# Performance work log

Hardware: AMD Instinct MI355X
Metric: run time of the kernel (lower is better)

Reference implementation:

```python
import jax, jax.numpy as jnp
import numpy as np

T, N, C, D, S = 512, 32, 1296, 512, 30
NORM_SCALE = 32.0
NEGINF = -1e9


def setup_inputs() -> dict:
    key = jax.random.key(0)
    k1, k2, k3, k4, k5 = jax.random.split(key, 5)
    feats = jax.random.normal(k1, (T * N, D), dtype=jnp.float32)
    classifier_weight = jax.random.normal(k2, (D, C), dtype=jnp.float32)
    labeling = jax.random.randint(k3, (N, S), 1, C)  # targets cannot be blank(0)
    logit_lgts = (T - jax.random.randint(k4, (N,), 0, 32)).astype(jnp.int32)
    labeling_lgts = (S - jax.random.randint(k5, (N,), 0, 5)).astype(jnp.int32)
    return dict(feats=feats, classifier_weight=classifier_weight,
                labeling=labeling, logit_lgts=logit_lgts, labeling_lgts=labeling_lgts)


def _ctc_loss(log_probs, labels, in_lens, lab_lens):
    # log_probs: (T, N, C); labels: (N, S); blank = 0; reduction = 'sum'
    Tt, Nn, Cc = log_probs.shape
    Ss = labels.shape[1]
    L = 2 * Ss + 1
    # extended labeling: blank, l1, blank, l2, ..., blank  -> (N, L)
    ext = jnp.zeros((Nn, L), dtype=labels.dtype).at[:, 1::2].set(labels)
    # gather per-state log-probs: (T, N, L)
    lp_ext = jnp.take_along_axis(log_probs, jnp.broadcast_to(ext[None], (Tt, Nn, L)), axis=2)
    # skip transition s-2 -> s allowed iff s > 1 and ext[s] != ext[s-2]
    skip_ok = jnp.concatenate(
        [jnp.zeros((Nn, 2), dtype=bool), ext[:, 2:] != ext[:, :-2]], axis=1)
    alpha0 = (jnp.full((Nn, L), NEGINF, dtype=log_probs.dtype)
              .at[:, 0].set(lp_ext[0, :, 0])
              .at[:, 1].set(lp_ext[0, :, 1]))

    def step(alpha, inp):
        lp_t, t = inp  # lp_t: (N, L)
        a1 = alpha
        a2 = jnp.pad(alpha[:, :-1], ((0, 0), (1, 0)), constant_values=NEGINF)
        a3 = jnp.where(skip_ok,
                       jnp.pad(alpha[:, :-2], ((0, 0), (2, 0)), constant_values=NEGINF),
                       NEGINF)
        new = jax.nn.logsumexp(jnp.stack([a1, a2, a3], axis=0), axis=0) + lp_t
        # freeze alpha once t reaches a sample's input length
        alpha = jnp.where((t < in_lens)[:, None], new, alpha)
        return alpha, None

    alpha, _ = jax.lax.scan(step, alpha0, (lp_ext[1:], jnp.arange(1, Tt)))
    Ln = 2 * lab_lens + 1  # (N,)
    last = jnp.take_along_axis(alpha, (Ln - 1)[:, None], axis=1)[:, 0]
    last2 = jnp.take_along_axis(alpha, (Ln - 2)[:, None], axis=1)[:, 0]
    nll = -jnp.logaddexp(last, last2)
    return jnp.sum(nll)


def reference(feats, classifier_weight, labeling, logit_lgts, labeling_lgts):
    # RadialCTC: cosine logits with norm_scale, then CTC on log-softmax.
    w_n = classifier_weight / jnp.linalg.norm(classifier_weight, axis=0, keepdims=True)  # (D, C)
    f_n = feats / jnp.linalg.norm(feats, axis=1, keepdims=True)  # (T*N, D)
    logits = NORM_SCALE * (f_n @ w_n)  # (T*N, C)
    log_probs = jax.nn.log_softmax(logits.reshape(T, N, C), axis=-1)
    return _ctc_loss(log_probs, labeling, logit_lgts, labeling_lgts)
```

## Files before the change

kernel.cpp:

```cpp
#include <hip/hip_runtime.h>
#include <stdint.h>
#include <stddef.h>


typedef _Float16 f16;
typedef _Float16 f16x8 __attribute__((ext_vector_type(8)));
typedef float f32x4 __attribute__((ext_vector_type(4)));
typedef __attribute__((address_space(1))) void* as1_void_ptr;
typedef __attribute__((address_space(3))) void* as3_void_ptr;

#define TT 512
#define NN 32
#define CC 1296
#define DD 512
#define SS 30
#define CP 1408
#define LL 61
#define NORM_SCALE 32.0f
#define LOG2E 1.4426950408889634f
#define LN2   0.6931471805599453f

#define PREP_WBLK (CP / 16)
#define PREP_ZBLK 16
#define PREP_FBLK (TT * NN / 4)

#define GEMM_BLK ((TT * NN / 128) * (CP / 128))
#define MEGA_GC  NN
#define MEGA_BLK (MEGA_GC + GEMM_BLK)

__device__ __forceinline__ float fexp2(float x) { return __builtin_amdgcn_exp2f(x); }
__device__ __forceinline__ float flog2(float x) { return __builtin_amdgcn_logf(x); }

__device__ __forceinline__ double dpp_sr1_zero64(double x) {
    long long b = __double_as_longlong(x);
    int lo = (int)(b & 0xFFFFFFFFLL);
    int hi = (int)(b >> 32);
    int lo2 = __builtin_amdgcn_update_dpp(0, lo, 0x138, 0xF, 0xF, false);
    int hi2 = __builtin_amdgcn_update_dpp(0, hi, 0x138, 0xF, 0xF, false);
    return __longlong_as_double(((long long)hi2 << 32) |
                                (unsigned long long)(unsigned int)lo2);
}
template <int CTRL>
__device__ __forceinline__ int dpp_imax_level(int m) {
    int t = __builtin_amdgcn_update_dpp(0, m, CTRL, 0xF, 0xF, false);
    return m > t ? m : t;
}

__global__ __launch_bounds__(256) void prep_kernel(const float* __restrict__ W,
                                                   const float* __restrict__ feats,
                                                   f16* __restrict__ wt,
                                                   f16* __restrict__ fn,
                                                   float* __restrict__ sumexp) {
    int bx = blockIdx.x, tid = threadIdx.x;
    if (bx < PREP_WBLK) {
        __shared__ float red[256];
        __shared__ float rqs[16];
        int c0 = bx * 16;
        int cl = tid & 15, dg = tid >> 4;
        int c = c0 + cl;
        float ss = 0.f;
        if (c < CC) {
            for (int d = dg; d < DD; d += 16) {
                float v = W[(size_t)d * CC + c];
                ss += v * v;
            }
        }
        red[tid] = ss;
        __syncthreads();
        if (tid < 16) {
            float s2 = 0.f;
            #pragma unroll
            for (int k = 0; k < 16; ++k) s2 += red[tid + 16 * k];
            rqs[tid] = rsqrtf(s2);
        }
        __syncthreads();
        int c_loc = tid >> 4, dl = tid & 15;
        int cc = c0 + c_loc;
        float rq = rqs[c_loc];
        #pragma unroll 4
        for (int it = 0; it < 32; ++it) {
            int d = dl + it * 16;
            float v = (cc < CC) ? W[(size_t)d * CC + cc] * rq : 0.f;
            wt[(size_t)cc * DD + d] = (f16)v;
        }
    } else if (bx < PREP_WBLK + PREP_ZBLK) {
        int zb = bx - PREP_WBLK;
        float4 z = {0.f, 0.f, 0.f, 0.f};
        ((float4*)sumexp)[zb * 256 + tid] = z;
    } else {
        int fb = bx - PREP_WBLK - PREP_ZBLK;
        int wv = (fb * 256 + tid) >> 6;
        int lane = tid & 63;
        const float4* src = (const float4*)(feats + (size_t)wv * DD) + lane * 2;
        float4 a = src[0], b = src[1];
        float ss = a.x*a.x + a.y*a.y + a.z*a.z + a.w*a.w
                 + b.x*b.x + b.y*b.y + b.z*b.z + b.w*b.w;
        #pragma unroll
        for (int off = 32; off; off >>= 1) ss += __shfl_xor(ss, off);
        float r = rsqrtf(ss);
        f16x8 o;
        o[0]=(f16)(a.x*r); o[1]=(f16)(a.y*r); o[2]=(f16)(a.z*r); o[3]=(f16)(a.w*r);
        o[4]=(f16)(b.x*r); o[5]=(f16)(b.y*r); o[6]=(f16)(b.z*r); o[7]=(f16)(b.w*r);
        *(f16x8*)(fn + (size_t)wv * DD + lane * 8) = o;
    }
}

template <int NT>
__device__ __forceinline__ void gather_wave(const f16* __restrict__ A,
                                            const f16* __restrict__ B,
                                            const int* __restrict__ labels,
                                            float* __restrict__ lp_lab,
                                            int n, int rbase, int lane) {
    __builtin_amdgcn_s_setprio(2);
    int lm = lane & 15, hi = lane >> 4;
    int cls0 = (lm == 0) ? 0 : labels[n * SS + lm - 1];
    int cls1 = (lm >= 15) ? 0 : labels[n * SS + lm + 15];
    const f16* pb0 = B + (size_t)cls0 * DD + hi * 8;
    const f16* pb1 = B + (size_t)cls1 * DD + hi * 8;
    const f16* pa0 = A + ((size_t)(rbase + lm) * NN + n) * DD + hi * 8;
    for (int c = 0; c < 4; ++c) {
        f32x4 acc[NT][2];
        #pragma unroll
        for (int i = 0; i < NT; ++i) {
            acc[i][0] = (f32x4){0.f, 0.f, 0.f, 0.f};
            acc[i][1] = (f32x4){0.f, 0.f, 0.f, 0.f};
        }
        const f16* pac = pa0 + (size_t)c * 128 * NN * DD;
        for (int kb = 0; kb < 16; ++kb) {
            f16x8 bf0 = *(const f16x8*)(pb0 + kb * 32);
            f16x8 bf1 = *(const f16x8*)(pb1 + kb * 32);
            #pragma unroll
            for (int i = 0; i < NT; ++i) {
                f16x8 af = *(const f16x8*)(pac + (size_t)(i * 16) * NN * DD + kb * 32);
                acc[i][0] = __builtin_amdgcn_mfma_f32_16x16x32_f16(af, bf0, acc[i][0], 0, 0, 0);
                acc[i][1] = __builtin_amdgcn_mfma_f32_16x16x32_f16(af, bf1, acc[i][1], 0, 0, 0);
            }
        }
        #pragma unroll
        for (int i = 0; i < NT; ++i) {
            #pragma unroll
            for (int jn = 0; jn < 2; ++jn) {
                int jc = jn * 16 + lm;
                if (jc >= 31) continue;
                float4 o;
                o.x = acc[i][jn][0] * (NORM_SCALE * LOG2E);
                o.y = acc[i][jn][1] * (NORM_SCALE * LOG2E);
                o.z = acc[i][jn][2] * (NORM_SCALE * LOG2E);
                o.w = acc[i][jn][3] * (NORM_SCALE * LOG2E);
                *(float4*)&lp_lab[((size_t)n * 31 + jc) * TT
                                  + c * 128 + rbase + i * 16 + hi * 4] = o;
            }
        }
        __syncthreads();
    }
    __builtin_amdgcn_s_setprio(0);
}

__global__ __launch_bounds__(256) void mega_kernel(const f16* __restrict__ A,
                                                   const f16* __restrict__ B,
                                                   const int* __restrict__ labels,
                                                   const int* __restrict__ in_lens,
                                                   const int* __restrict__ lab_lens,
                                                   float* __restrict__ sumexp,
                                                   float* __restrict__ lp_lab,
                                                   double* __restrict__ part) {
    __shared__ __align__(16) f16 sm[8192];
    int bx = blockIdx.x;
    int tid = threadIdx.x;
    int w = tid >> 6, lane = tid & 63;
    int lm = lane & 15, hi = lane >> 4;
    int sw = (lm >> 1) & 3;

    if (bx >= MEGA_GC) {
        int j = bx - MEGA_GC;
        int x = j & 7, rr = j >> 3;
        int bm = x * 16 + (rr & 15);
        int bn = rr >> 4;
        int wm = w >> 1, wn = w & 1;
        f32x4 acc[4][4];
        f32x4 zero = {0.f, 0.f, 0.f, 0.f};
        #pragma unroll
        for (int i = 0; i < 4; ++i)
            #pragma unroll
            for (int jj = 0; jj < 4; ++jj) acc[i][jj] = zero;

        for (int kb = 0; kb < 16; ++kb) {
            #pragma unroll
            for (int p = 0; p < 2; ++p) {
                int s = p * 256 + tid;
                int row = s >> 2;
                int ch = (s & 3) ^ ((row >> 1) & 3);
                const f16* ga = A + (size_t)(bm * 128 + row) * DD + kb * 32 + ch * 8;
                const f16* gb = B + (size_t)(bn * 128 + row) * DD + kb * 32 + ch * 8;
                __builtin_amdgcn_global_load_lds((as1_void_ptr)ga,
                    (as3_void_ptr)&sm[(p * 256 + w * 64) * 8], 16, 0, 0);
                __builtin_amdgcn_global_load_lds((as1_void_ptr)gb,
                    (as3_void_ptr)&sm[4096 + (p * 256 + w * 64) * 8], 16, 0, 0);
            }
            __syncthreads();
            f16x8 af[4], bf[4];
            #pragma unroll
            for (int i = 0; i < 4; ++i)
                af[i] = *(const f16x8*)&sm[(wm * 64 + i * 16 + lm) * 32 + (hi ^ sw) * 8];
            #pragma unroll
            for (int jj = 0; jj < 4; ++jj)
                bf[jj] = *(const f16x8*)&sm[4096 + (wn * 64 + jj * 16 + lm) * 32 + (hi ^ sw) * 8];
            #pragma unroll
            for (int i = 0; i < 4; ++i)
                #pragma unroll
                for (int jj = 0; jj < 4; ++jj)
                    acc[i][jj] = __builtin_amdgcn_mfma_f32_16x16x32_f16(af[i], bf[jj], acc[i][jj], 0, 0, 0);
            __syncthreads();
        }
        #pragma unroll
        for (int i = 0; i < 4; ++i) {
            float rs[4] = {0.f, 0.f, 0.f, 0.f};
            #pragma unroll
            for (int jj = 0; jj < 4; ++jj) {
                int c = bn * 128 + wn * 64 + jj * 16 + lm;
                bool ok = (c < CC);
                #pragma unroll
                for (int r = 0; r < 4; ++r)
                    rs[r] += ok ? fexp2(acc[i][jj][r] * (NORM_SCALE * LOG2E)) : 0.f;
            }
            #pragma unroll
            for (int off = 1; off < 16; off <<= 1) {
                #pragma unroll
                for (int r = 0; r < 4; ++r) rs[r] += __shfl_xor(rs[r], off);
            }
            if (lm == 0) {
                int rowb = bm * 128 + wm * 64 + i * 16 + hi * 4;
                #pragma unroll
                for (int r = 0; r < 4; ++r) atomicAdd(&sumexp[rowb + r], rs[r]);
            }
        }
        return;
    }

    int n = bx;
    if (w > 0) {
        if (w < 3) gather_wave<3>(A, B, labels, lp_lab, n, (w - 1) * 48, lane);
        else       gather_wave<2>(A, B, labels, lp_lab, n, 96, lane);
        return;
    }

    int s = lane;
    bool valid = s < LL;
    int ext = (valid && (s & 1)) ? labels[n * SS + (s >> 1)] : 0;
    int jmap = (valid && (s & 1)) ? ((s >> 1) + 1) : 0;
    int ext2 = __shfl_up(ext, 2);
    double skipd = ((s >= 2) && valid && (ext != ext2)) ? 1.0 : 0.0;
    double sk1 = dpp_sr1_zero64(skipd);
    double sk2 = dpp_sr1_zero64(sk1);
    double kk2 = skipd * sk2;
    int Tin = in_lens[n];
    const float4* g4 = (const float4*)(lp_lab + ((size_t)n * 31 + jmap) * TT);

    double beta = 0.0;
    int Mi = 0;

    auto stepL = [&](float lp) {
        double P = (double)fexp2(lp);
        double b1 = dpp_sr1_zero64(beta);
        double b2 = dpp_sr1_zero64(b1);
        beta = (beta + b1 + b2 * skipd) * P;
    };
    auto step2 = [&](float lp1, float lp2) {
        double q  = (double)fexp2(lp1);
        double P2 = (double)fexp2(lp2);
        double q1 = dpp_sr1_zero64(q);
        double q2 = dpp_sr1_zero64(q1);
        double c1 = q + q1;
        double c2 = fma(skipd, q + q2, q1);
        double c3 = fma(sk1, q1, skipd * q2);
        double c4 = kk2 * q2;
        double b1 = dpp_sr1_zero64(beta);
        double b2 = dpp_sr1_zero64(b1);
        double b3 = dpp_sr1_zero64(b2);
        double b4 = dpp_sr1_zero64(b3);
        double u = fma(c1, b1, q * beta);
        double v = fma(c3, b3, c2 * b2);
        beta = (u + fma(c4, b4, v)) * P2;
    };
    auto renorm = [&]() {
        int h = (int)(__double_as_longlong(beta) >> 32);
        h = dpp_imax_level<0x111>(h);
        h = dpp_imax_level<0x112>(h);
        h = dpp_imax_level<0x114>(h);
        h = dpp_imax_level<0x118>(h);
        int r0 = __builtin_amdgcn_readlane(h, 15);
        int r1 = __builtin_amdgcn_readlane(h, 31);
        int r2 = __builtin_amdgcn_readlane(h, 47);
        int r3 = __builtin_amdgcn_readlane(h, 63);
        int mx = max(max(r0, r1), max(r2, r3));
        int e11 = mx >> 20;
        double scale = __longlong_as_double((long long)(2046 - e11) << 52);
        beta *= scale;
        Mi += e11 - 1023;
    };

    __builtin_amdgcn_s_setprio(3);
    __syncthreads();
    float4 a0 = g4[0], a1 = g4[1];
    float4 pc0 = g4[2], pc1 = g4[3];
    float4 pn0 = g4[4], pn1 = g4[5];
    beta = (s <= 1) ? (double)fexp2(a0.x) : 0.0;

    stepL(a0.y); stepL(a0.z); stepL(a0.w);
    stepL(a1.x); stepL(a1.y); stepL(a1.z); stepL(a1.w);
    renorm();
    int remaining = Tin - 8;
    int g = 2;
    int rn = 0;
    for (int c = 0; c < 4; ++c) {
        if (c > 0) {
            __syncthreads();
            pc0 = g4[g];     pc1 = g4[g + 1];
            pn0 = g4[g + 2]; pn1 = g4[g + 3];
        }
        int gend = 32 * (c + 1);
        while (g + 2 <= gend && remaining >= 8) {
            int i0 = g + 4 > 127 ? 127 : g + 4;
            int i1 = g + 5 > 127 ? 127 : g + 5;
            float4 pp0 = g4[i0], pp1 = g4[i1];
            step2(pc0.x, pc0.y); step2(pc0.z, pc0.w);
            step2(pc1.x, pc1.y); step2(pc1.z, pc1.w);
            rn ^= 1;
            if (!rn) renorm();
            pc0 = pn0; pc1 = pn1; pn0 = pp0; pn1 = pp1;
            remaining -= 8; g += 2;
        }
    }
    if (remaining > 0) stepL(pc0.x);
    if (remaining > 1) stepL(pc0.y);
    if (remaining > 2) stepL(pc0.z);
    if (remaining > 3) stepL(pc0.w);
    if (remaining > 4) stepL(pc1.x);
    if (remaining > 5) stepL(pc1.y);
    if (remaining > 6) stepL(pc1.z);
    __builtin_amdgcn_s_setprio(0);

    int Ln = 2 * lab_lens[n] + 1;
    double last  = __shfl(beta, Ln - 1);
    double last2 = __shfl(beta, Ln - 2);
    double smv = last + last2;
    long long bb = __double_as_longlong(smv);
    int e = (int)(bb >> 52) - 1023;
    double mant = __longlong_as_double((bb & 0xFFFFFFFFFFFFFLL) | (1023LL << 52));
    if (s == 0)
        part[n] = (double)flog2((float)mant) + (double)(e + Mi);
}

__global__ __launch_bounds__(1024) void final_kernel(const float* __restrict__ sumexp,
                                                     const int* __restrict__ in_lens,
                                                     const double* __restrict__ part,
                                                     float* __restrict__ out) {
    int tid = threadIdx.x;
    int v = tid >> 6, lane = tid & 63;
    __shared__ float nl[NN];
    #pragma unroll
    for (int k = 0; k < 2; ++k) {
        int n = v * 2 + k;
        int Tin = in_lens[n];
        double ms = 0.0;
        for (int t = lane; t < Tin; t += 64)
            ms += (double)flog2(sumexp[(size_t)t * NN + n]);
        #pragma unroll
        for (int off = 32; off; off >>= 1) ms += __shfl_xor(ms, off);
        if (lane == 0) nl[n] = (float)(-(part[n] - ms) * LN2);
    }
    __syncthreads();
    if (tid == 0) {
        float t = 0.f;
        for (int i = 0; i < NN; ++i) t += nl[i];
        out[0] = t;
    }
}

extern "C" void kernel_launch(void* const* d_in, const int* in_sizes, int n_in,
                              void* d_out, int out_size, void* d_ws, size_t ws_size,
                              hipStream_t stream) {
    const float* feats        = (const float*)d_in[0];
    const float* W            = (const float*)d_in[1];
    const int*   labeling     = (const int*)d_in[2];
    const int*   logit_lgts   = (const int*)d_in[3];
    const int*   labeling_lgts= (const int*)d_in[4];
    float* out = (float*)d_out;
    char* ws = (char*)d_ws;

    size_t off = 0;
    f16*   wt     = (f16*)(ws + off);   off += (size_t)CP * DD * 2;
    f16*   fn     = (f16*)(ws + off);   off += (size_t)TT * NN * DD * 2;
    float* sumexp = (float*)(ws + off); off += (size_t)TT * NN * 4;
    float* lp_lab = (float*)(ws + off); off += (size_t)NN * 31 * TT * 4;
    double* part  = (double*)(ws + off); off += NN * 8;

    prep_kernel<<<PREP_WBLK + PREP_ZBLK + PREP_FBLK, 256, 0, stream>>>(
        W, feats, wt, fn, sumexp);
    mega_kernel<<<MEGA_BLK, 256, 0, stream>>>(fn, wt, labeling, logit_lgts,
                                              labeling_lgts, sumexp, lp_lab, part);
    final_kernel<<<1, 1024, 0, stream>>>(sumexp, logit_lgts, part, out);

    (void)in_sizes; (void)n_in; (void)out_size; (void)ws_size;
}
```

Baseline: 153.2 us.

## Split CTC recursion into concurrent forward and backward halves meeting at midpoint

The serial CTC alpha recursion over all timesteps now runs on two waves per sample. One wave does the forward pass over t<256 and another does a backward (beta) pass from Tin-1 down to 256; the two are combined by a dot product through shared memory. The gather work shrinks to two waves that process 128-row chunks in the order the two recursions consume them, and the syncs are rearranged to match. This roughly halves the critical serial dependency chain, at the cost of more complex synchronisation and a second scaled recursion that has to be renormalised.

```diff
diff --git a/kernel.cpp b/kernel.cpp
--- a/kernel.cpp
+++ b/kernel.cpp
@@ -40,10 +40,39 @@
     return __longlong_as_double(((long long)hi2 << 32) |
                                 (unsigned long long)(unsigned int)lo2);
 }
+__device__ __forceinline__ double dpp_sl1_zero64(double x) {
+    long long b = __double_as_longlong(x);
+    int lo = (int)(b & 0xFFFFFFFFLL);
+    int hi = (int)(b >> 32);
+    int lo2 = __builtin_amdgcn_update_dpp(0, lo, 0x130, 0xF, 0xF, false);
+    int hi2 = __builtin_amdgcn_update_dpp(0, hi, 0x130, 0xF, 0xF, false);
+    return __longlong_as_double(((long long)hi2 << 32) |
+                                (unsigned long long)(unsigned int)lo2);
+}
+__device__ __forceinline__ float dpp_sl1_zero32(float x) {
+    int r = __builtin_amdgcn_update_dpp(0, __float_as_int(x), 0x130, 0xF, 0xF, false);
+    return __int_as_float(r);
+}
 template <int CTRL>
 __device__ __forceinline__ int dpp_imax_level(int m) {
     int t = __builtin_amdgcn_update_dpp(0, m, CTRL, 0xF, 0xF, false);
     return m > t ? m : t;
+}
+__device__ __forceinline__ void renorm_d(double& x, int& Mi) {
+    int h = (int)(__double_as_longlong(x) >> 32);
+    h = dpp_imax_level<0x111>(h);
+    h = dpp_imax_level<0x112>(h);
+    h = dpp_imax_level<0x114>(h);
+    h = dpp_imax_level<0x118>(h);
+    int r0 = __builtin_amdgcn_readlane(h, 15);
+    int r1 = __builtin_amdgcn_readlane(h, 31);
+    int r2 = __builtin_amdgcn_readlane(h, 47);
+    int r3 = __builtin_amdgcn_readlane(h, 63);
+    int mx = max(max(r0, r1), max(r2, r3));
+    int e11 = mx >> 20;
+    double scale = __longlong_as_double((long long)(2046 - e11) << 52);
+    x *= scale;
+    Mi += e11 - 1023;
 }
 
 __global__ __launch_bounds__(256) void prep_kernel(const float* __restrict__ W,
@@ -106,54 +135,44 @@
 }
 
 template <int NT>
-__device__ __forceinline__ void gather_wave(const f16* __restrict__ A,
-                                            const f16* __restrict__ B,
-                                            const int* __restrict__ labels,
-                                            float* __restrict__ lp_lab,
-                                            int n, int rbase, int lane) {
-    __builtin_amdgcn_s_setprio(2);
+__device__ __forceinline__ void gather_chunk(const f16* __restrict__ pb0,
+                                             const f16* __restrict__ pb1,
+                                             const f16* __restrict__ A,
+                                             float* __restrict__ lp_lab,
+                                             int n, int c, int rbase, int lane) {
     int lm = lane & 15, hi = lane >> 4;
-    int cls0 = (lm == 0) ? 0 : labels[n * SS + lm - 1];
-    int cls1 = (lm >= 15) ? 0 : labels[n * SS + lm + 15];
-    const f16* pb0 = B + (size_t)cls0 * DD + hi * 8;
-    const f16* pb1 = B + (size_t)cls1 * DD + hi * 8;
-    const f16* pa0 = A + ((size_t)(rbase + lm) * NN + n) * DD + hi * 8;
-    for (int c = 0; c < 4; ++c) {
-        f32x4 acc[NT][2];
+    const f16* pa0 = A + ((size_t)(c * 128 + rbase + lm) * NN + n) * DD + hi * 8;
+    f32x4 acc[NT][2];
+    #pragma unroll
+    for (int i = 0; i < NT; ++i) {
+        acc[i][0] = (f32x4){0.f, 0.f, 0.f, 0.f};
+        acc[i][1] = (f32x4){0.f, 0.f, 0.f, 0.f};
+    }
+    for (int kb = 0; kb < 16; ++kb) {
+        f16x8 bf0 = *(const f16x8*)(pb0 + kb * 32);
+        f16x8 bf1 = *(const f16x8*)(pb1 + kb * 32);
         #pragma unroll
         for (int i = 0; i < NT; ++i) {
-            acc[i][0] = (f32x4){0.f, 0.f, 0.f, 0.f};
-            acc[i][1] = (f32x4){0.f, 0.f, 0.f, 0.f};
-        }
-        const f16* pac = pa0 + (size_t)c * 128 * NN * DD;
-        for (int kb = 0; kb < 16; ++kb) {
-            f16x8 bf0 = *(const f16x8*)(pb0 + kb * 32);
-            f16x8 bf1 = *(const f16x8*)(pb1 + kb * 32);
-            #pragma unroll
-            for (int i = 0; i < NT; ++i) {
-                f16x8 af = *(const f16x8*)(pac + (size_t)(i * 16) * NN * DD + kb * 32);
-                acc[i][0] = __builtin_amdgcn_mfma_f32_16x16x32_f16(af, bf0, acc[i][0], 0, 0, 0);
-                acc[i][1] = __builtin_amdgcn_mfma_f32_16x16x32_f16(af, bf1, acc[i][1], 0, 0, 0);
-            }
-        }
-        #pragma unroll
-        for (int i = 0; i < NT; ++i) {
-            #pragma unroll
-            for (int jn = 0; jn < 2; ++jn) {
-                int jc = jn * 16 + lm;
-                if (jc >= 31) continue;
-                float4 o;
-                o.x = acc[i][jn][0] * (NORM_SCALE * LOG2E);
-                o.y = acc[i][jn][1] * (NORM_SCALE * LOG2E);
-                o.z = acc[i][jn][2] * (NORM_SCALE * LOG2E);
-                o.w = acc[i][jn][3] * (NORM_SCALE * LOG2E);
-                *(float4*)&lp_lab[((size_t)n * 31 + jc) * TT
-                                  + c * 128 + rbase + i * 16 + hi * 4] = o;
-            }
-        }
-        __syncthreads();
-    }
-    __builtin_amdgcn_s_setprio(0);
+            f16x8 af = *(const f16x8*)(pa0 + (size_t)(i * 16) * NN * DD + kb * 32);
+            acc[i][0] = __builtin_amdgcn_mfma_f32_16x16x32_f16(af, bf0, acc[i][0], 0, 0, 0);
+            acc[i][1] = __builtin_amdgcn_mfma_f32_16x16x32_f16(af, bf1, acc[i][1], 0, 0, 0);
+        }
+    }
+    #pragma unroll
+    for (int i = 0; i < NT; ++i) {
+        #pragma unroll
+        for (int jn = 0; jn < 2; ++jn) {
+            int jc = jn * 16 + lm;
+            if (jc >= 31) continue;
+            float4 o;
+            o.x = acc[i][jn][0] * (NORM_SCALE * LOG2E);
+            o.y = acc[i][jn][1] * (NORM_SCALE * LOG2E);
+            o.z = acc[i][jn][2] * (NORM_SCALE * LOG2E);
+            o.w = acc[i][jn][3] * (NORM_SCALE * LOG2E);
+            *(float4*)&lp_lab[((size_t)n * 31 + jc) * TT
+                              + c * 128 + rbase + i * 16 + hi * 4] = o;
+        }
+    }
 }
 
 __global__ __launch_bounds__(256) void mega_kernel(const f16* __restrict__ A,
@@ -238,9 +257,22 @@
     }
 
     int n = bx;
-    if (w > 0) {
-        if (w < 3) gather_wave<3>(A, B, labels, lp_lab, n, (w - 1) * 48, lane);
-        else       gather_wave<2>(A, B, labels, lp_lab, n, 96, lane);
+    if (w >= 2) {
+        __builtin_amdgcn_s_setprio(2);
+        int cls0 = (lm == 0) ? 0 : labels[n * SS + lm - 1];
+        int cls1 = (lm >= 15) ? 0 : labels[n * SS + lm + 15];
+        const f16* pb0 = B + (size_t)cls0 * DD + hi * 8;
+        const f16* pb1 = B + (size_t)cls1 * DD + hi * 8;
+        int cA = (w == 2) ? 0 : 3;
+        int cB = (w == 2) ? 1 : 2;
+        gather_chunk<4>(pb0, pb1, A, lp_lab, n, cA, 0, lane);
+        gather_chunk<4>(pb0, pb1, A, lp_lab, n, cA, 64, lane);
+        __syncthreads();
+        gather_chunk<4>(pb0, pb1, A, lp_lab, n, cB, 0, lane);
+        gather_chunk<4>(pb0, pb1, A, lp_lab, n, cB, 64, lane);
+        __builtin_amdgcn_s_setprio(0);
+        __syncthreads();
+        __syncthreads();
         return;
     }
 
@@ -248,107 +280,158 @@
     bool valid = s < LL;
     int ext = (valid && (s & 1)) ? labels[n * SS + (s >> 1)] : 0;
     int jmap = (valid && (s & 1)) ? ((s >> 1) + 1) : 0;
-    int ext2 = __shfl_up(ext, 2);
-    double skipd = ((s >= 2) && valid && (ext != ext2)) ? 1.0 : 0.0;
-    double sk1 = dpp_sr1_zero64(skipd);
-    double sk2 = dpp_sr1_zero64(sk1);
-    double kk2 = skipd * sk2;
     int Tin = in_lens[n];
-    const float4* g4 = (const float4*)(lp_lab + ((size_t)n * 31 + jmap) * TT);
-
-    double beta = 0.0;
-    int Mi = 0;
-
-    auto stepL = [&](float lp) {
-        double P = (double)fexp2(lp);
-        double b1 = dpp_sr1_zero64(beta);
-        double b2 = dpp_sr1_zero64(b1);
-        beta = (beta + b1 + b2 * skipd) * P;
-    };
-    auto step2 = [&](float lp1, float lp2) {
-        double q  = (double)fexp2(lp1);
-        double P2 = (double)fexp2(lp2);
-        double q1 = dpp_sr1_zero64(q);
-        double q2 = dpp_sr1_zero64(q1);
-        double c1 = q + q1;
-        double c2 = fma(skipd, q + q2, q1);
-        double c3 = fma(sk1, q1, skipd * q2);
-        double c4 = kk2 * q2;
-        double b1 = dpp_sr1_zero64(beta);
-        double b2 = dpp_sr1_zero64(b1);
-        double b3 = dpp_sr1_zero64(b2);
-        double b4 = dpp_sr1_zero64(b3);
-        double u = fma(c1, b1, q * beta);
-        double v = fma(c3, b3, c2 * b2);
-        beta = (u + fma(c4, b4, v)) * P2;
-    };
-    auto renorm = [&]() {
-        int h = (int)(__double_as_longlong(beta) >> 32);
-        h = dpp_imax_level<0x111>(h);
-        h = dpp_imax_level<0x112>(h);
-        h = dpp_imax_level<0x114>(h);
-        h = dpp_imax_level<0x118>(h);
-        int r0 = __builtin_amdgcn_readlane(h, 15);
-        int r1 = __builtin_amdgcn_readlane(h, 31);
-        int r2 = __builtin_amdgcn_readlane(h, 47);
-        int r3 = __builtin_amdgcn_readlane(h, 63);
-        int mx = max(max(r0, r1), max(r2, r3));
-        int e11 = mx >> 20;
-        double scale = __longlong_as_double((long long)(2046 - e11) << 52);
-        beta *= scale;
-        Mi += e11 - 1023;
-    };
-
-    __builtin_amdgcn_s_setprio(3);
-    __syncthreads();
-    float4 a0 = g4[0], a1 = g4[1];
-    float4 pc0 = g4[2], pc1 = g4[3];
-    float4 pn0 = g4[4], pn1 = g4[5];
-    beta = (s <= 1) ? (double)fexp2(a0.x) : 0.0;
-
-    stepL(a0.y); stepL(a0.z); stepL(a0.w);
-    stepL(a1.x); stepL(a1.y); stepL(a1.z); stepL(a1.w);
-    renorm();
-    int remaining = Tin - 8;
-    int g = 2;
-    int rn = 0;
-    for (int c = 0; c < 4; ++c) {
-        if (c > 0) {
-            __syncthreads();
-            pc0 = g4[g];     pc1 = g4[g + 1];
-            pn0 = g4[g + 2]; pn1 = g4[g + 3];
-        }
-        int gend = 32 * (c + 1);
-        while (g + 2 <= gend && remaining >= 8) {
-            int i0 = g + 4 > 127 ? 127 : g + 4;
-            int i1 = g + 5 > 127 ? 127 : g + 5;
-            float4 pp0 = g4[i0], pp1 = g4[i1];
-            step2(pc0.x, pc0.y); step2(pc0.z, pc0.w);
-            step2(pc1.x, pc1.y); step2(pc1.z, pc1.w);
-            rn ^= 1;
-            if (!rn) renorm();
-            pc0 = pn0; pc1 = pn1; pn0 = pp0; pn1 = pp1;
-            remaining -= 8; g += 2;
-        }
-    }
-    if (remaining > 0) stepL(pc0.x);
-    if (remaining > 1) stepL(pc0.y);
-    if (remaining > 2) stepL(pc0.z);
-    if (remaining > 3) stepL(pc0.w);
-    if (remaining > 4) stepL(pc1.x);
-    if (remaining > 5) stepL(pc1.y);
-    if (remaining > 6) stepL(pc1.z);
-    __builtin_amdgcn_s_setprio(0);
-
-    int Ln = 2 * lab_lens[n] + 1;
-    double last  = __shfl(beta, Ln - 1);
-    double last2 = __shfl(beta, Ln - 2);
-    double smv = last + last2;
-    long long bb = __double_as_longlong(smv);
-    int e = (int)(bb >> 52) - 1023;
-    double mant = __longlong_as_double((bb & 0xFFFFFFFFFFFFFLL) | (1023LL << 52));
-    if (s == 0)
-        part[n] = (double)flog2((float)mant) + (double)(e + Mi);
+    const float* lpr = lp_lab + ((size_t)n * 31 + jmap) * TT;
+    double* vb = (double*)sm;
+
+    if (w == 0) {
+        int ext2 = __shfl_up(ext, 2);
+        double skipd = ((s >= 2) && valid && (ext != ext2)) ? 1.0 : 0.0;
+        double sk1 = dpp_sr1_zero64(skipd);
+        double sk2 = dpp_sr1_zero64(sk1);
+        double kk2 = skipd * sk2;
+        const float4* g4 = (const float4*)lpr;
+        double beta = 0.0;
+        int Mif = 0;
+
+        auto stepL = [&](float lp) {
+            double P = (double)fexp2(lp);
+            double b1 = dpp_sr1_zero64(beta);
+            double b2 = dpp_sr1_zero64(b1);
+            beta = (beta + b1 + b2 * skipd) * P;
+        };
+        auto step2 = [&](float lp1, float lp2) {
+            double q  = (double)fexp2(lp1);
+            double P2 = (double)fexp2(lp2);
+            double q1 = dpp_sr1_zero64(q);
+            double q2 = dpp_sr1_zero64(q1);
+            double c1 = q + q1;
+            double c2 = fma(skipd, q + q2, q1);
+            double c3 = fma(sk1, q1, skipd * q2);
+            double c4 = kk2 * q2;
+            double b1 = dpp_sr1_zero64(beta);
+            double b2 = dpp_sr1_zero64(b1);
+            double b3 = dpp_sr1_zero64(b2);
+            double b4 = dpp_sr1_zero64(b3);
+            double u = fma(c1, b1, q * beta);
+            double v2 = fma(c3, b3, c2 * b2);
+            beta = (u + fma(c4, b4, v2)) * P2;
+        };
+
+        __builtin_amdgcn_s_setprio(3);
+        __syncthreads();
+        float4 q0 = g4[0];
+        beta = (s <= 1) ? (double)fexp2(q0.x) : 0.0;
+        stepL(q0.y); stepL(q0.z); stepL(q0.w);
+        renorm_d(beta, Mif);
+        float4 cu = g4[1];
+        for (int gi = 1; gi <= 31; ++gi) {
+            float4 nx = g4[gi < 31 ? gi + 1 : 31];
+            step2(cu.x, cu.y); step2(cu.z, cu.w);
+            if (gi & 1) renorm_d(beta, Mif);
+            cu = nx;
+        }
+        __syncthreads();
+        cu = g4[32];
+        for (int gi = 32; gi <= 63; ++gi) {
+            float4 nx = g4[gi < 63 ? gi + 1 : 63];
+            step2(cu.x, cu.y); step2(cu.z, cu.w);
+            if (gi & 1) renorm_d(beta, Mif);
+            cu = nx;
+        }
+        renorm_d(beta, Mif);
+        __syncthreads();
+        __builtin_amdgcn_s_setprio(0);
+        double pr = beta * vb[s];
+        #pragma unroll
+        for (int off = 32; off; off >>= 1) pr += __shfl_xor(pr, off);
+        if (s == 0) {
+            long long bb = __double_as_longlong(pr);
+            int e = (int)(bb >> 52) - 1023;
+            double mant = __longlong_as_double((bb & 0xFFFFFFFFFFFFFLL) | (1023LL << 52));
+            part[n] = (double)flog2((float)mant) + (double)(e + Mif) + vb[64];
+        }
+        return;
+    }
+
+    {
+        float maskf = valid ? 1.f : 0.f;
+        int extd1 = __shfl_down(ext, 1);
+        int extd2 = __shfl_down(ext, 2);
+        int extd3 = __shfl_down(ext, 3);
+        int extd4 = __shfl_down(ext, 4);
+        double k2d = ((s + 2) < LL && extd2 != ext)   ? 1.0 : 0.0;
+        double k3d = ((s + 3) < LL && extd3 != extd1) ? 1.0 : 0.0;
+        double k4d = ((s + 4) < LL && extd4 != extd2) ? 1.0 : 0.0;
+        int Ln = 2 * lab_lens[n] + 1;
+        double v = (s == Ln - 1 || s == Ln - 2) ? 1.0 : 0.0;
+        int Mib = 0;
+
+        auto step2b = [&](float lph, float lpl) {
+            float p  = maskf * fexp2(lph);
+            float rr = maskf * fexp2(lpl);
+            float p1 = dpp_sl1_zero32(p);
+            float p2 = dpp_sl1_zero32(p1);
+            float p3 = dpp_sl1_zero32(p2);
+            float p4 = dpp_sl1_zero32(p3);
+            float r1 = dpp_sl1_zero32(rr);
+            float r2 = dpp_sl1_zero32(r1);
+            double rd = (double)rr, rd1 = (double)r1, rd2 = (double)r2;
+            double c0 = (double)p * rd;
+            double c1 = (double)p1 * (rd + rd1);
+            double c2 = (double)p2 * fma(k2d, rd + rd2, rd1);
+            double c3 = (double)p3 * fma(k3d, rd1, k2d * rd2);
+            double c4 = (double)p4 * (k2d * rd2) * k4d;
+            double v1 = dpp_sl1_zero64(v);
+            double v2 = dpp_sl1_zero64(v1);
+            double v3 = dpp_sl1_zero64(v2);
+            double v4 = dpp_sl1_zero64(v3);
+            double u  = fma(c1, v1, c0 * v);
+            double t2 = fma(c3, v3, c2 * v2);
+            v = u + fma(c4, v4, t2);
+        };
+        auto step1b = [&](float lph) {
+            float p = maskf * fexp2(lph);
+            double u  = (double)p * v;
+            double u1 = dpp_sl1_zero64(u);
+            double u2 = dpp_sl1_zero64(u1);
+            v = u + u1 + k2d * u2;
+        };
+
+        __builtin_amdgcn_s_setprio(3);
+        __syncthreads();
+        int tc = Tin - 1;
+        float h0 = lpr[tc], l0 = lpr[tc - 1];
+        int rnc = 0;
+        while (tc >= 385) {
+            int tn = tc - 2;
+            float h1 = (tn >= 384) ? lpr[tn] : 0.f;
+            float l1 = (tn >= 385) ? lpr[tn - 1] : 0.f;
+            step2b(h0, l0);
+            if (((++rnc) & 3) == 0) renorm_d(v, Mib);
+            tc = tn; h0 = h1; l0 = l1;
+        }
+        if (tc == 384) { step1b(h0); tc = 383; }
+        renorm_d(v, Mib);
+        __syncthreads();
+        tc = 383;
+        h0 = lpr[tc]; l0 = lpr[tc - 1];
+        rnc = 0;
+        while (tc >= 257) {
+            int tn = tc - 2;
+            float h1 = (tn >= 257) ? lpr[tn] : 0.f;
+            float l1 = (tn >= 257) ? lpr[tn - 1] : 0.f;
+            step2b(h0, l0);
+            if (((++rnc) & 3) == 0) renorm_d(v, Mib);
+            tc = tn; h0 = h1; l0 = l1;
+        }
+        renorm_d(v, Mib);
+        vb[s] = v;
+        if (s == 0) vb[64] = (double)Mib;
+        __builtin_amdgcn_s_setprio(0);
+        __syncthreads();
+        return;
+    }
 }
 
 __global__ __launch_bounds__(1024) void final_kernel(const float* __restrict__ sumexp,
```

Result: slower. 168.5 us (+10.1%).

## Stream label log-probs from gather waves to CTC wave through LDS

Applied to the files above, without the earlier changes.

The gather waves now write each 128-timestep chunk of per-label scaled logits into a shared-memory buffer instead of a global lp_lab array. The CTC recursion wave reads them from LDS, using a two-barrier handshake per chunk so the next chunk is not written until the current one has been consumed. This removes the global write/read round trip and its workspace, with the aim of cutting load latency on the serial CTC critical path. In exchange, gather compute is now strictly interlocked with CTC consumption chunk by chunk, which could stall the producers. The renormalisation lambda also moves into a helper function, and the prologue and chunk loop are restructured.

```diff
diff --git a/kernel.cpp b/kernel.cpp
--- a/kernel.cpp
+++ b/kernel.cpp
@@ -19,6 +19,7 @@
 #define NORM_SCALE 32.0f
 #define LOG2E 1.4426950408889634f
 #define LN2   0.6931471805599453f
+#define LPS_STRIDE 132
 
 #define PREP_WBLK (CP / 16)
 #define PREP_ZBLK 16
@@ -44,6 +45,22 @@
 __device__ __forceinline__ int dpp_imax_level(int m) {
     int t = __builtin_amdgcn_update_dpp(0, m, CTRL, 0xF, 0xF, false);
     return m > t ? m : t;
+}
+__device__ __forceinline__ void renorm_d(double& x, int& Mi) {
+    int h = (int)(__double_as_longlong(x) >> 32);
+    h = dpp_imax_level<0x111>(h);
+    h = dpp_imax_level<0x112>(h);
+    h = dpp_imax_level<0x114>(h);
+    h = dpp_imax_level<0x118>(h);
+    int r0 = __builtin_amdgcn_readlane(h, 15);
+    int r1 = __builtin_amdgcn_readlane(h, 31);
+    int r2 = __builtin_amdgcn_readlane(h, 47);
+    int r3 = __builtin_amdgcn_readlane(h, 63);
+    int mx = max(max(r0, r1), max(r2, r3));
+    int e11 = mx >> 20;
+    double scale = __longlong_as_double((long long)(2046 - e11) << 52);
+    x *= scale;
+    Mi += e11 - 1023;
 }
 
 __global__ __launch_bounds__(256) void prep_kernel(const float* __restrict__ W,
@@ -106,18 +123,14 @@
 }
 
 template <int NT>
-__device__ __forceinline__ void gather_wave(const f16* __restrict__ A,
-                                            const f16* __restrict__ B,
-                                            const int* __restrict__ labels,
-                                            float* __restrict__ lp_lab,
+__device__ __forceinline__ void gather_pipe(f16* sm,
+                                            const f16* __restrict__ pb0,
+                                            const f16* __restrict__ pb1,
+                                            const f16* __restrict__ A,
                                             int n, int rbase, int lane) {
-    __builtin_amdgcn_s_setprio(2);
     int lm = lane & 15, hi = lane >> 4;
-    int cls0 = (lm == 0) ? 0 : labels[n * SS + lm - 1];
-    int cls1 = (lm >= 15) ? 0 : labels[n * SS + lm + 15];
-    const f16* pb0 = B + (size_t)cls0 * DD + hi * 8;
-    const f16* pb1 = B + (size_t)cls1 * DD + hi * 8;
-    const f16* pa0 = A + ((size_t)(rbase + lm) * NN + n) * DD + hi * 8;
+    float* lps = (float*)sm;
+    #pragma unroll 1
     for (int c = 0; c < 4; ++c) {
         f32x4 acc[NT][2];
         #pragma unroll
@@ -125,17 +138,18 @@
             acc[i][0] = (f32x4){0.f, 0.f, 0.f, 0.f};
             acc[i][1] = (f32x4){0.f, 0.f, 0.f, 0.f};
         }
-        const f16* pac = pa0 + (size_t)c * 128 * NN * DD;
+        const f16* pa0 = A + ((size_t)(c * 128 + rbase + lm) * NN + n) * DD + hi * 8;
         for (int kb = 0; kb < 16; ++kb) {
             f16x8 bf0 = *(const f16x8*)(pb0 + kb * 32);
             f16x8 bf1 = *(const f16x8*)(pb1 + kb * 32);
             #pragma unroll
             for (int i = 0; i < NT; ++i) {
-                f16x8 af = *(const f16x8*)(pac + (size_t)(i * 16) * NN * DD + kb * 32);
+                f16x8 af = *(const f16x8*)(pa0 + (size_t)(i * 16) * NN * DD + kb * 32);
                 acc[i][0] = __builtin_amdgcn_mfma_f32_16x16x32_f16(af, bf0, acc[i][0], 0, 0, 0);
                 acc[i][1] = __builtin_amdgcn_mfma_f32_16x16x32_f16(af, bf1, acc[i][1], 0, 0, 0);
             }
         }
+        __syncthreads();
         #pragma unroll
         for (int i = 0; i < NT; ++i) {
             #pragma unroll
@@ -147,13 +161,11 @@
                 o.y = acc[i][jn][1] * (NORM_SCALE * LOG2E);
                 o.z = acc[i][jn][2] * (NORM_SCALE * LOG2E);
                 o.w = acc[i][jn][3] * (NORM_SCALE * LOG2E);
-                *(float4*)&lp_lab[((size_t)n * 31 + jc) * TT
-                                  + c * 128 + rbase + i * 16 + hi * 4] = o;
-            }
-        }
-        __syncthreads();
-    }
-    __builtin_amdgcn_s_setprio(0);
+                *(float4*)&lps[jc * LPS_STRIDE + rbase + i * 16 + hi * 4] = o;
+            }
+        }
+        __syncthreads();
+    }
 }
 
 __global__ __launch_bounds__(256) void mega_kernel(const f16* __restrict__ A,
@@ -162,7 +174,6 @@
                                                    const int* __restrict__ in_lens,
                                                    const int* __restrict__ lab_lens,
                                                    float* __restrict__ sumexp,
-                                                   float* __restrict__ lp_lab,
                                                    double* __restrict__ part) {
     __shared__ __align__(16) f16 sm[8192];
     int bx = blockIdx.x;
@@ -238,9 +249,15 @@
     }
 
     int n = bx;
-    if (w > 0) {
-        if (w < 3) gather_wave<3>(A, B, labels, lp_lab, n, (w - 1) * 48, lane);
-        else       gather_wave<2>(A, B, labels, lp_lab, n, 96, lane);
+    if (w >= 1) {
+        __builtin_amdgcn_s_setprio(2);
+        int cls0 = (lm == 0) ? 0 : labels[n * SS + lm - 1];
+        int cls1 = (lm >= 15) ? 0 : labels[n * SS + lm + 15];
+        const f16* pb0 = B + (size_t)cls0 * DD + hi * 8;
+        const f16* pb1 = B + (size_t)cls1 * DD + hi * 8;
+        if (w < 3) gather_pipe<3>(sm, pb0, pb1, A, n, (w - 1) * 48, lane);
+        else       gather_pipe<2>(sm, pb0, pb1, A, n, 96, lane);
+        __builtin_amdgcn_s_setprio(0);
         return;
     }
 
@@ -248,16 +265,16 @@
     bool valid = s < LL;
     int ext = (valid && (s & 1)) ? labels[n * SS + (s >> 1)] : 0;
     int jmap = (valid && (s & 1)) ? ((s >> 1) + 1) : 0;
+    int Tin = in_lens[n];
     int ext2 = __shfl_up(ext, 2);
     double skipd = ((s >= 2) && valid && (ext != ext2)) ? 1.0 : 0.0;
     double sk1 = dpp_sr1_zero64(skipd);
     double sk2 = dpp_sr1_zero64(sk1);
     double kk2 = skipd * sk2;
-    int Tin = in_lens[n];
-    const float4* g4 = (const float4*)(lp_lab + ((size_t)n * 31 + jmap) * TT);
+    const float4* row4 = (const float4*)((float*)sm + jmap * LPS_STRIDE);
 
     double beta = 0.0;
-    int Mi = 0;
+    int Mif = 0;
 
     auto stepL = [&](float lp) {
         double P = (double)fexp2(lp);
@@ -279,65 +296,49 @@
         double b3 = dpp_sr1_zero64(b2);
         double b4 = dpp_sr1_zero64(b3);
         double u = fma(c1, b1, q * beta);
-        double v = fma(c3, b3, c2 * b2);
-        beta = (u + fma(c4, b4, v)) * P2;
+        double v2 = fma(c3, b3, c2 * b2);
+        beta = (u + fma(c4, b4, v2)) * P2;
     };
-    auto renorm = [&]() {
-        int h = (int)(__double_as_longlong(beta) >> 32);
-        h = dpp_imax_level<0x111>(h);
-        h = dpp_imax_level<0x112>(h);
-        h = dpp_imax_level<0x114>(h);
-        h = dpp_imax_level<0x118>(h);
-        int r0 = __builtin_amdgcn_readlane(h, 15);
-        int r1 = __builtin_amdgcn_readlane(h, 31);
-        int r2 = __builtin_amdgcn_readlane(h, 47);
-        int r3 = __builtin_amdgcn_readlane(h, 63);
-        int mx = max(max(r0, r1), max(r2, r3));
-        int e11 = mx >> 20;
-        double scale = __longlong_as_double((long long)(2046 - e11) << 52);
-        beta *= scale;
-        Mi += e11 - 1023;
-    };
 
     __builtin_amdgcn_s_setprio(3);
-    __syncthreads();
-    float4 a0 = g4[0], a1 = g4[1];
-    float4 pc0 = g4[2], pc1 = g4[3];
-    float4 pn0 = g4[4], pn1 = g4[5];
-    beta = (s <= 1) ? (double)fexp2(a0.x) : 0.0;
-
-    stepL(a0.y); stepL(a0.z); stepL(a0.w);
-    stepL(a1.x); stepL(a1.y); stepL(a1.z); stepL(a1.w);
-    renorm();
-    int remaining = Tin - 8;
-    int g = 2;
-    int rn = 0;
+    int remaining = Tin - 1;
+    int rnc = 0;
+    #pragma unroll 1
     for (int c = 0; c < 4; ++c) {
-        if (c > 0) {
-            __syncthreads();
-            pc0 = g4[g];     pc1 = g4[g + 1];
-            pn0 = g4[g + 2]; pn1 = g4[g + 3];
-        }
-        int gend = 32 * (c + 1);
-        while (g + 2 <= gend && remaining >= 8) {
-            int i0 = g + 4 > 127 ? 127 : g + 4;
-            int i1 = g + 5 > 127 ? 127 : g + 5;
-            float4 pp0 = g4[i0], pp1 = g4[i1];
-            step2(pc0.x, pc0.y); step2(pc0.z, pc0.w);
-            step2(pc1.x, pc1.y); step2(pc1.z, pc1.w);
-            rn ^= 1;
-            if (!rn) renorm();
-            pc0 = pn0; pc1 = pn1; pn0 = pp0; pn1 = pp1;
-            remaining -= 8; g += 2;
-        }
-    }
-    if (remaining > 0) stepL(pc0.x);
-    if (remaining > 1) stepL(pc0.y);
-    if (remaining > 2) stepL(pc0.z);
-    if (remaining > 3) stepL(pc0.w);
-    if (remaining > 4) stepL(pc1.x);
-    if (remaining > 5) stepL(pc1.y);
-    if (remaining > 6) stepL(pc1.z);
+        __syncthreads();
+        __syncthreads();
+        if (c == 0) {
+            float4 q0 = row4[0];
+            beta = (s <= 1) ? (double)fexp2(q0.x) : 0.0;
+            stepL(q0.y); stepL(q0.z); stepL(q0.w);
+            renorm_d(beta, Mif);
+            remaining -= 3;
+            float4 cu = row4[1];
+            for (int gi = 1; gi <= 31; ++gi) {
+                float4 nx = row4[gi < 31 ? gi + 1 : 31];
+                step2(cu.x, cu.y); step2(cu.z, cu.w);
+                if (gi & 1) renorm_d(beta, Mif);
+                cu = nx;
+            }
+            remaining -= 124;
+        } else {
+            float4 cu = row4[0];
+            int gi = 0;
+            while (remaining >= 4 && gi <= 31) {
+                float4 nx = row4[gi < 31 ? gi + 1 : 31];
+                step2(cu.x, cu.y); step2(cu.z, cu.w);
+                rnc ^= 1;
+                if (!rnc) renorm_d(beta, Mif);
+                cu = nx; remaining -= 4; ++gi;
+            }
+            if (c == 3) {
+                if (remaining > 0) stepL(cu.x);
+                if (remaining > 1) stepL(cu.y);
+                if (remaining > 2) stepL(cu.z);
+            }
+        }
+    }
+    renorm_d(beta, Mif);
     __builtin_amdgcn_s_setprio(0);
 
     int Ln = 2 * lab_lens[n] + 1;
@@ -348,7 +349,7 @@
     int e = (int)(bb >> 52) - 1023;
     double mant = __longlong_as_double((bb & 0xFFFFFFFFFFFFFLL) | (1023LL << 52));
     if (s == 0)
-        part[n] = (double)flog2((float)mant) + (double)(e + Mi);
+        part[n] = (double)flog2((float)mant) + (double)(e + Mif);
 }
 
 __global__ __launch_bounds__(1024) void final_kernel(const float* __restrict__ sumexp,
@@ -392,13 +393,12 @@
     f16*   wt     = (f16*)(ws + off);   off += (size_t)CP * DD * 2;
     f16*   fn     = (f16*)(ws + off);   off += (size_t)TT * NN * DD * 2;
     float* sumexp = (float*)(ws + off); off += (size_t)TT * NN * 4;
-    float* lp_lab = (float*)(ws + off); off += (size_t)NN * 31 * TT * 4;
     double* part  = (double*)(ws + off); off += NN * 8;
 
     prep_kernel<<<PREP_WBLK + PREP_ZBLK + PREP_FBLK, 256, 0, stream>>>(
         W, feats, wt, fn, sumexp);
     mega_kernel<<<MEGA_BLK, 256, 0, stream>>>(fn, wt, labeling, logit_lgts,
-                                              labeling_lgts, sumexp, lp_lab, part);
+                                              labeling_lgts, sumexp, part);
     final_kernel<<<1, 1024, 0, stream>>>(sumexp, logit_lgts, part, out);
 
     (void)in_sizes; (void)n_in; (void)out_size; (void)ws_size;
```

Measured after the change: 149.5 us. -2.4%, faster.
